# Performance work log

Measured on AMD Instinct MI355X. Metric: run time of the kernel, lower is better.

The kernel has to match this reference:

```python
import jax, jax.numpy as jnp
import numpy as np

N, C, A = 4096, 1000, 64


def setup_inputs() -> dict:
    key = jax.random.key(0)
    k1, k2, k3, k4, k5 = jax.random.split(key, 5)
    weight_m = jax.random.normal(k1, (C, A), dtype=jnp.float32)
    y = jax.random.normal(k2, (N, C), dtype=jnp.float32)
    features = jax.random.normal(k3, (N, A), dtype=jnp.float32)
    target_x = jax.random.randint(k4, (N,), 0, C)
    ratio = jnp.float32(0.5)
    final_conv = jax.random.normal(k5, (N, A, A), dtype=jnp.float32) * 0.1
    return {
        "weight_m": weight_m,
        "y": y,
        "features": features,
        "target_x": target_x,
        "ratio": ratio,
        "final_conv": final_conv,
        "class_num": C,
    }


def reference(weight_m, y, features, target_x, ratio, final_conv, class_num):
    # weight_m: (C, A); y: (N, C); features: (N, A) (only supplies N, A)
    # target_x: (N,) int labels; final_conv: (N, A, A); ratio: scalar
    Wk = weight_m[target_x]                       # (N, A)  gather of label row
    d = weight_m[None, :, :] - Wk[:, None, :]     # (N, C, A) = NxW_ij - NxW_kj

    # sigma1 = ||w_j||^2 - ||w_{y_n}||^2
    w2 = jnp.sum(weight_m * weight_m, axis=-1)    # (C,)
    sigma1 = w2[None, :] - w2[target_x][:, None]  # (N, C)

    # sigma2 = ratio * diag(d @ CV @ d^T), computed directly (no NxCxC matrix)
    t = jnp.einsum('nca,nab->ncb', d, final_conv)  # (N, C, A)
    sigma2 = ratio * jnp.sum(t * d, axis=-1)       # (N, C)

    logits = y + 0.5 * sigma2 + sigma1             # (N, C)

    # mean cross-entropy (nn.CrossEntropyLoss default)
    logp = jax.nn.log_softmax(logits, axis=-1)
    nll = -jnp.take_along_axis(logp, target_x[:, None], axis=1)[:, 0]
    loss = jnp.mean(nll)
    return loss, y
```

## Files before the change

### kernel.cpp

```cpp
#include <hip/hip_runtime.h>
#include <hip/hip_bf16.h>
#include <stdint.h>
#include <stddef.h>

#define N_    4096
#define C_    1000
#define CP    1024
#define A_    64
#define KPACK 2080
#define KCROSS (KPACK + 64)
#define KTOT  2176
#define KSPLIT 1152
#define MS    68

typedef __bf16 bf16_8 __attribute__((ext_vector_type(8)));
typedef float  f32_4  __attribute__((ext_vector_type(4)));

__device__ __forceinline__ void gl2lds16(const void* g, void* l) {
  __builtin_amdgcn_global_load_lds(
      (const __attribute__((address_space(1))) void*)g,
      (__attribute__((address_space(3))) void*)l, 16, 0, 0);
}

__device__ __forceinline__ uint16_t pk_fp8(float a, float b) {
  return (uint16_t)(__builtin_amdgcn_cvt_pk_fp8_f32(a, b, 0, false) & 0xffff);
}

__device__ __forceinline__ void unpack_pair(int k, int& a, int& b) {
  a = (int)(0.5f * (129.0f - sqrtf((float)(16641 - 8 * k))));
  if (a < 0) a = 0;
  while ((a + 1) * (129 - (a + 1)) / 2 <= k) ++a;
  while (a * (129 - a) / 2 > k) --a;
  b = k - a * (129 - a) / 2 + a;
}

__global__ __launch_bounds__(256) void prep_all(
    const float* __restrict__ W, const int* __restrict__ tgt,
    const float* __restrict__ CV, uint8_t* __restrict__ Bo,
    float* __restrict__ w2, uint8_t* __restrict__ Aq, float* __restrict__ qn) {
  __shared__ float Ms[64 * MS];
  __shared__ float up[4 * 64];
  __shared__ float wk[64];
  __shared__ float us[64];
  int t = threadIdx.x;

  if (blockIdx.x < 1024) {
    int c = blockIdx.x;
    float* ws = Ms;
    if (t < 64) {
      float w = (c < C_) ? W[c * 64 + t] : 0.f;
      ws[t] = w;
      float s = w * w;
      for (int o = 32; o; o >>= 1) s += __shfl_down(s, o);
      if (t == 0 && c < C_) w2[c] = s;
    }
    __syncthreads();
    uint8_t* row = Bo + (size_t)c * KTOT;
    for (int p = t; p < KPACK / 2; p += 256) {
      int k = 2 * p;
      int a0, b0, a1, b1;
      unpack_pair(k, a0, b0);
      if (b0 == 63) { a1 = a0 + 1; b1 = a1; } else { a1 = a0; b1 = b0 + 1; }
      *(uint16_t*)(row + k) = pk_fp8(ws[a0] * ws[b0], ws[a1] * ws[b1]);
    }
    if (t < 32) *(uint16_t*)(row + KPACK + 2 * t) = pk_fp8(ws[2 * t], ws[2 * t + 1]);
    if (t >= 32 && t < 48) *(uint16_t*)(row + KCROSS + 2 * (t - 32)) = 0;
  } else {
    int n = blockIdx.x - 1024;
    int lbl = tgt[n];
    if (t < 64) wk[t] = W[lbl * 64 + t];
    const float4* M4 = (const float4*)(CV + (size_t)n * 4096);
    for (int j = 0; j < 4; ++j) {
      int i4 = t + j * 256;
      int r = i4 >> 4, c4 = (i4 & 15) << 2;
      *(float4*)&Ms[r * MS + c4] = M4[i4];
    }
    __syncthreads();
    {
      int a = t & 63, seg = t >> 6;
      float acc = 0.f;
      for (int b = seg * 16; b < seg * 16 + 16; ++b)
        acc += (Ms[a * MS + b] + Ms[b * MS + a]) * wk[b];
      up[seg * 64 + a] = acc;
    }
    __syncthreads();
    if (t < 64) {
      float u = up[t] + up[64 + t] + up[128 + t] + up[192 + t];
      us[t] = u;
      float p = wk[t] * u;
      for (int o = 32; o; o >>= 1) p += __shfl_down(p, o);
      if (t == 0) qn[n] = 0.5f * p;
    }
    __syncthreads();
    uint8_t* row = Aq + (size_t)n * KTOT;
    for (int p = t; p < KPACK / 2; p += 256) {
      int k = 2 * p;
      int a0, b0, a1, b1;
      unpack_pair(k, a0, b0);
      if (b0 == 63) { a1 = a0 + 1; b1 = a1; } else { a1 = a0; b1 = b0 + 1; }
      float v0 = (a0 == b0) ? Ms[a0 * MS + a0] : (Ms[a0 * MS + b0] + Ms[b0 * MS + a0]);
      float v1 = (a1 == b1) ? Ms[a1 * MS + a1] : (Ms[a1 * MS + b1] + Ms[b1 * MS + a1]);
      *(uint16_t*)(row + k) = pk_fp8(v0, v1);
    }
    if (t < 32) *(uint16_t*)(row + KPACK + 2 * t) = pk_fp8(-us[2 * t], -us[2 * t + 1]);
    if (t >= 32 && t < 48) *(uint16_t*)(row + KCROSS + 2 * (t - 32)) = 0;
  }
}

#define BM 128
#define BN 128
#define BK 128
__global__ __launch_bounds__(256) void gemm_s(const uint8_t* __restrict__ Aq,
                                              const uint8_t* __restrict__ Bo,
                                              __bf16* __restrict__ Sbase) {
  __shared__ uint8_t As[BM * BK];
  __shared__ uint8_t Bs[BN * BK];
  int t = threadIdx.x;
  int lane = t & 63;
  int w = t >> 6;
  int wr = w & 1;
  int wc = w >> 1;
  int rowBase = blockIdx.x * BM;
  int colBase = blockIdx.y * BN;
  int kb = blockIdx.z ? KSPLIT : 0;
  int ke = blockIdx.z ? KTOT : KSPLIT;
  __bf16* S = Sbase + (size_t)blockIdx.z * ((size_t)N_ * CP);

  f32_4 acc[4][4];
  for (int mi = 0; mi < 4; ++mi)
    for (int ni = 0; ni < 4; ++ni)
      acc[mi][ni] = (f32_4){0.f, 0.f, 0.f, 0.f};

  int m0 = lane & 15;
  int q = lane >> 4;
  int sw = m0 & 7;

  for (int k0 = kb; k0 < ke; k0 += BK) {
    __syncthreads();
    for (int r = 0; r < 4; ++r) {
      int ch = r * 256 + t;
      int row_p = ch >> 3, qp = ch & 7;
      int q_log = qp ^ (row_p & 7);
      const uint8_t* g = Aq + (size_t)(rowBase + row_p) * KTOT + k0 + (q_log << 4);
      gl2lds16(g, As + ch * 16);
    }
    for (int r = 0; r < 4; ++r) {
      int ch = r * 256 + t;
      int row_p = ch >> 3, qp = ch & 7;
      int q_log = qp ^ (row_p & 7);
      const uint8_t* g = Bo + (size_t)(colBase + row_p) * KTOT + k0 + (q_log << 4);
      gl2lds16(g, Bs + ch * 16);
    }
    __syncthreads();
    for (int s = 0; s < 4; ++s) {
      int c_log = 2 * s + (q >> 1);
      int off = ((c_log ^ sw) << 4) + ((q & 1) << 3);
      long af[4], bf[4];
      for (int mi = 0; mi < 4; ++mi)
        af[mi] = *(const long*)&As[(wr * 64 + mi * 16 + m0) * BK + off];
      for (int ni = 0; ni < 4; ++ni)
        bf[ni] = *(const long*)&Bs[(wc * 64 + ni * 16 + m0) * BK + off];
      for (int mi = 0; mi < 4; ++mi)
        for (int ni = 0; ni < 4; ++ni)
          acc[mi][ni] = __builtin_amdgcn_mfma_f32_16x16x32_fp8_fp8(
              af[mi], bf[ni], acc[mi][ni], 0, 0, 0);
    }
  }

  int ccol = lane & 15;
  int rrow = (lane >> 4) * 4;
  for (int mi = 0; mi < 4; ++mi)
    for (int ni = 0; ni < 4; ++ni) {
      int r0 = rowBase + wr * 64 + mi * 16 + rrow;
      int c0 = colBase + wc * 64 + ni * 16 + ccol;
      for (int j = 0; j < 4; ++j)
        S[(size_t)(r0 + j) * CP + c0] = (__bf16)acc[mi][ni][j];
    }
}

__global__ __launch_bounds__(256) void epilogue(
    const __bf16* __restrict__ Sb, const float* __restrict__ y,
    const float* __restrict__ w2, const float* __restrict__ qn,
    const int* __restrict__ tgt, const float* __restrict__ ratio_p,
    float* __restrict__ nll, float* __restrict__ outy) {
  int t = threadIdx.x, lane = t & 63, w = t >> 6;
  int n = blockIdx.x * 4 + w;
  float hr = 0.5f * (*ratio_p);
  int lbl = tgt[n];
  float q = qn[n];
  float w2k = w2[lbl];
  const bf16_8* S0 = (const bf16_8*)(Sb + (size_t)n * CP);
  const bf16_8* S1 = (const bf16_8*)(Sb + 1ull * N_ * CP + (size_t)n * CP);
  const float* yr = y + (size_t)n * C_;
  float* oy = outy + (size_t)n * C_;
  float l[16];
  float mx = -1e30f;
  for (int i = 0; i < 2; ++i) {
    int idx = i * 64 + lane;
    bf16_8 a0 = S0[idx], a1 = S1[idx];
    int c0 = idx * 8;
    for (int j = 0; j < 8; ++j) {
      int c = c0 + j;
      float v = -1e30f;
      if (c < C_) {
        float s = (float)a0[j] + (float)a1[j];
        v = yr[c] + (w2[c] - w2k) + hr * (s + q);
      }
      l[i * 8 + j] = v;
      mx = fmaxf(mx, v);
    }
  }
  for (int c = lane; c < C_; c += 64) oy[c] = yr[c];
  for (int o = 32; o; o >>= 1) mx = fmaxf(mx, __shfl_xor(mx, o));
  float se = 0.f, lt = 0.f;
  for (int i = 0; i < 2; ++i) {
    int c0 = (i * 64 + lane) * 8;
    for (int j = 0; j < 8; ++j) {
      float v = l[i * 8 + j];
      se += expf(v - mx);
      lt += (c0 + j == lbl) ? v : 0.f;
    }
  }
  for (int o = 32; o; o >>= 1) {
    se += __shfl_xor(se, o);
    lt += __shfl_xor(lt, o);
  }
  if (lane == 0) nll[n] = (mx + logf(se)) - lt;
}

__global__ void reduce_loss(const float* __restrict__ nll, float* __restrict__ out) {
  int t = threadIdx.x;
  float s = 0.f;
  for (int i = t; i < N_; i += 256) s += nll[i];
  for (int o = 32; o; o >>= 1) s += __shfl_down(s, o);
  __shared__ float r[4];
  if ((t & 63) == 0) r[t >> 6] = s;
  __syncthreads();
  if (t == 0) out[0] = (r[0] + r[1] + r[2] + r[3]) * (1.0f / (float)N_);
}

extern "C" void kernel_launch(void* const* d_in, const int* in_sizes, int n_in,
                              void* d_out, int out_size, void* d_ws, size_t ws_size,
                              hipStream_t stream) {
  const float* W     = (const float*)d_in[0];
  const float* y     = (const float*)d_in[1];
  const int*   tgt   = (const int*)d_in[3];
  const float* ratio = (const float*)d_in[4];
  const float* CV    = (const float*)d_in[5];

  char* ws = (char*)d_ws;
  size_t off = 0;
  uint8_t* Aq = (uint8_t*)(ws + off); off += (size_t)N_ * KTOT;
  uint8_t* Bo = (uint8_t*)(ws + off); off += (size_t)CP * KTOT;
  __bf16* S   = (__bf16*)(ws + off);  off += 2ull * N_ * CP * sizeof(__bf16);
  float* w2   = (float*)(ws + off);   off += 4096;
  float* qn   = (float*)(ws + off);   off += (size_t)N_ * sizeof(float);
  float* nll  = (float*)(ws + off);   off += (size_t)N_ * sizeof(float);

  float* out = (float*)d_out;

  prep_all<<<1024 + N_, 256, 0, stream>>>(W, tgt, CV, Bo, w2, Aq, qn);
  gemm_s<<<dim3(N_ / BM, CP / BN, 2), 256, 0, stream>>>(Aq, Bo, S);
  epilogue<<<N_ / 4, 256, 0, stream>>>(S, y, w2, qn, tgt, ratio, nll, out + 1);
  reduce_loss<<<1, 256, 0, stream>>>(nll, out);
}
```

Baseline: 165.8 us.

## Overlap y passthrough copy with GEMM and vectorize transposed S stores

The copy of y to the output moves from the epilogue into the GEMM kernel. Each of the 512 GEMM blocks copies 8000 floats, spread in 1000-element chunks across its K iterations, so the copy traffic overlaps with MFMA work. The MFMA operands are also swapped so each lane holds four consecutive columns of one row, which lets the S tile be written as packed 8-byte bf16 stores instead of scattered 2-byte ones. The risk is that the extra global traffic inside the GEMM loop slows the matrix core pipeline.

```diff
diff --git a/kernel.cpp b/kernel.cpp
--- a/kernel.cpp
+++ b/kernel.cpp
@@ -12,6 +12,7 @@
 #define KTOT  2176
 #define KSPLIT 1152
 #define MS    68
+#define YPER  8000
 
 typedef __bf16 bf16_8 __attribute__((ext_vector_type(8)));
 typedef float  f32_4  __attribute__((ext_vector_type(4)));
@@ -112,7 +113,9 @@
 #define BK 128
 __global__ __launch_bounds__(256) void gemm_s(const uint8_t* __restrict__ Aq,
                                               const uint8_t* __restrict__ Bo,
-                                              __bf16* __restrict__ Sbase) {
+                                              __bf16* __restrict__ Sbase,
+                                              const float* __restrict__ y,
+                                              float* __restrict__ outy) {
   __shared__ uint8_t As[BM * BK];
   __shared__ uint8_t Bs[BN * BK];
   int t = threadIdx.x;
@@ -126,6 +129,10 @@
   int ke = blockIdx.z ? KTOT : KSPLIT;
   __bf16* S = Sbase + (size_t)blockIdx.z * ((size_t)N_ * CP);
 
+  int bid = blockIdx.x + 32 * blockIdx.y + 256 * blockIdx.z;
+  const float* ysrc = y + (size_t)bid * YPER;
+  float* ydst = outy + (size_t)bid * YPER;
+
   f32_4 acc[4][4];
   for (int mi = 0; mi < 4; ++mi)
     for (int ni = 0; ni < 4; ++ni)
@@ -135,6 +142,7 @@
   int q = lane >> 4;
   int sw = m0 & 7;
 
+  int it = 0;
   for (int k0 = kb; k0 < ke; k0 += BK) {
     __syncthreads();
     for (int r = 0; r < 4; ++r) {
@@ -150,6 +158,12 @@
       int q_log = qp ^ (row_p & 7);
       const uint8_t* g = Bo + (size_t)(colBase + row_p) * KTOT + k0 + (q_log << 4);
       gl2lds16(g, Bs + ch * 16);
+    }
+    {
+      int base = it * 1000;
+      ++it;
+      for (int i = base + t; i < base + 1000 && i < YPER; i += 256)
+        ydst[i] = ysrc[i];
     }
     __syncthreads();
     for (int s = 0; s < 4; ++s) {
@@ -163,26 +177,28 @@
       for (int mi = 0; mi < 4; ++mi)
         for (int ni = 0; ni < 4; ++ni)
           acc[mi][ni] = __builtin_amdgcn_mfma_f32_16x16x32_fp8_fp8(
-              af[mi], bf[ni], acc[mi][ni], 0, 0, 0);
-    }
-  }
-
-  int ccol = lane & 15;
-  int rrow = (lane >> 4) * 4;
-  for (int mi = 0; mi < 4; ++mi)
+              bf[ni], af[mi], acc[mi][ni], 0, 0, 0);
+    }
+  }
+
+  int ll = lane & 15;
+  int lh = lane >> 4;
+  for (int mi = 0; mi < 4; ++mi) {
+    int n0 = rowBase + wr * 64 + mi * 16 + ll;
     for (int ni = 0; ni < 4; ++ni) {
-      int r0 = rowBase + wr * 64 + mi * 16 + rrow;
-      int c0 = colBase + wc * 64 + ni * 16 + ccol;
-      for (int j = 0; j < 4; ++j)
-        S[(size_t)(r0 + j) * CP + c0] = (__bf16)acc[mi][ni][j];
-    }
+      int c0 = colBase + wc * 64 + ni * 16 + lh * 4;
+      union { __bf16 h[4]; uint2 u; } pk;
+      for (int j = 0; j < 4; ++j) pk.h[j] = (__bf16)acc[mi][ni][j];
+      *(uint2*)&S[(size_t)n0 * CP + c0] = pk.u;
+    }
+  }
 }
 
 __global__ __launch_bounds__(256) void epilogue(
     const __bf16* __restrict__ Sb, const float* __restrict__ y,
     const float* __restrict__ w2, const float* __restrict__ qn,
     const int* __restrict__ tgt, const float* __restrict__ ratio_p,
-    float* __restrict__ nll, float* __restrict__ outy) {
+    float* __restrict__ nll) {
   int t = threadIdx.x, lane = t & 63, w = t >> 6;
   int n = blockIdx.x * 4 + w;
   float hr = 0.5f * (*ratio_p);
@@ -192,7 +208,6 @@
   const bf16_8* S0 = (const bf16_8*)(Sb + (size_t)n * CP);
   const bf16_8* S1 = (const bf16_8*)(Sb + 1ull * N_ * CP + (size_t)n * CP);
   const float* yr = y + (size_t)n * C_;
-  float* oy = outy + (size_t)n * C_;
   float l[16];
   float mx = -1e30f;
   for (int i = 0; i < 2; ++i) {
@@ -210,7 +225,6 @@
       mx = fmaxf(mx, v);
     }
   }
-  for (int c = lane; c < C_; c += 64) oy[c] = yr[c];
   for (int o = 32; o; o >>= 1) mx = fmaxf(mx, __shfl_xor(mx, o));
   float se = 0.f, lt = 0.f;
   for (int i = 0; i < 2; ++i) {
@@ -260,7 +274,7 @@
   float* out = (float*)d_out;
 
   prep_all<<<1024 + N_, 256, 0, stream>>>(W, tgt, CV, Bo, w2, Aq, qn);
-  gemm_s<<<dim3(N_ / BM, CP / BN, 2), 256, 0, stream>>>(Aq, Bo, S);
-  epilogue<<<N_ / 4, 256, 0, stream>>>(S, y, w2, qn, tgt, ratio, nll, out + 1);
+  gemm_s<<<dim3(N_ / BM, CP / BN, 2), 256, 0, stream>>>(Aq, Bo, S, y, out + 1);
+  epilogue<<<N_ / 4, 256, 0, stream>>>(S, y, w2, qn, tgt, ratio, nll);
   reduce_loss<<<1, 256, 0, stream>>>(nll, out);
 }
```

Result: slower. 173.7 us (+4.7%).
